# Performance work log

Measured on AMD Instinct MI355X. Metric: run time of the kernel, lower is better.

## Reference

```python
import jax, jax.numpy as jnp
import numpy as np

N_NODES = 50000


def setup_inputs() -> dict:
    key = jax.random.key(0)
    ks = jax.random.split(key, 6)
    E = 640000
    H = 128
    data = jax.random.normal(ks[0], (N_NODES, H), dtype=jnp.float32)
    edge = jax.random.randint(ks[1], (2, E), 0, N_NODES, dtype=jnp.int64)
    att = jax.random.uniform(ks[2], (E,), dtype=jnp.float32)
    w1 = jax.random.normal(ks[3], (2 * H, H), dtype=jnp.float32) * (1.0 / np.sqrt(2 * H))
    b1 = jnp.zeros((H,), dtype=jnp.float32)
    w2 = jax.random.normal(ks[4], (2 * H, H), dtype=jnp.float32) * (1.0 / np.sqrt(2 * H))
    b2 = jnp.zeros((H,), dtype=jnp.float32)
    return {"data": data, "edge": edge, "att": att, "w1": w1, "b1": b1, "w2": w2, "b2": b2}


def _simple_conv_mean_cat(x, edge, att):
    # PyG SimpleConv(aggr='mean', combine_root='cat') with scalar edge weights.
    src, dst = edge[0], edge[1]
    msgs = x[src] * att[:, None]                               # [E, H] gather + scale
    summed = jax.ops.segment_sum(msgs, dst, num_segments=N_NODES)   # [N, H]
    deg = jax.ops.segment_sum(jnp.ones_like(att), dst, num_segments=N_NODES)  # [N]
    agg = summed / jnp.maximum(deg, 1.0)[:, None]              # mean over incoming edges
    return jnp.concatenate([x, agg], axis=-1)                  # [N, 2H]


def reference(data, edge, att, w1, b1, w2, b2):
    out = _simple_conv_mean_cat(data, edge, att)
    out = jax.nn.relu(out @ w1 + b1)
    out = _simple_conv_mean_cat(out, edge, att)
    out = jax.nn.relu(out @ w2 + b2)
    return out
```

## Files before the change

### kernel.cpp

```cpp
#include <hip/hip_runtime.h>


#define HDIM 128
#define CAP 32
#define FCH 2048

typedef __bf16 bf16x8 __attribute__((ext_vector_type(8)));
typedef float floatx4 __attribute__((ext_vector_type(4)));

__device__ __forceinline__ unsigned short f2bf(float f) {
    unsigned int u = __float_as_uint(f);
    unsigned int r = (u + 0x7fff + ((u >> 16) & 1)) >> 16;
    return (unsigned short)r;
}
__device__ __forceinline__ float bf2f(unsigned short b) {
    return __uint_as_float((unsigned int)b << 16);
}

__global__ __launch_bounds__(256) void k_fill(const int* __restrict__ edge, int E,
                                              const float* __restrict__ att,
                                              int* __restrict__ cursor,
                                              int* __restrict__ ovf_cnt,
                                              unsigned int* __restrict__ pse,
                                              float4* __restrict__ ovf, int rsize,
                                              int nfb,
                                              const float* __restrict__ data,
                                              unsigned short* __restrict__ data_bf, int n4,
                                              int cb, int NN,
                                              const float* __restrict__ w1,
                                              unsigned short* __restrict__ w1t,
                                              const float* __restrict__ w2,
                                              unsigned short* __restrict__ w2t) {
    int b = blockIdx.x;
    int t = threadIdx.x;
    if (b < nfb) {
        __shared__ int s_or;
        if (t == 0) s_or = 0;
        __syncthreads();
        int nw = 2 * E < 512 ? 2 * E : 512;
        int iw = t * 2 + 1;
        int vw = (iw < nw) ? edge[iw] : 0;
        if (vw != 0) atomicOr(&s_or, 1);
        __syncthreads();
        int sh = (s_or == 0) ? 1 : 0;

        int r = b & 7;
        int c = b >> 3;
        int lo = r * rsize;
        int hi = lo + rsize;
        int e0 = c * FCH;
        int ds[8];
#pragma unroll
        for (int k = 0; k < 8; ++k) {
            int e = e0 + t + k * 256;
            ds[k] = (e < E) ? edge[(size_t)(E + e) << sh] : -1;
        }
#pragma unroll
        for (int k = 0; k < 8; ++k) {
            int d = ds[k];
            if (d >= lo && d < hi) {
                int e = e0 + t + k * 256;
                int s = edge[(size_t)e << sh];
                float a = att[e];
                int slot = atomicAdd(&cursor[d], 1);
                if (slot < CAP) {
                    unsigned int rec = ((unsigned int)f2bf(a) << 16) | (unsigned int)(s & 0xffff);
                    pse[(size_t)d * CAP + slot] = rec;
                } else {
                    int oi = atomicAdd(ovf_cnt, 1);
                    ovf[oi] = make_float4(__int_as_float(d), __int_as_float(s), a, 0.f);
                }
            }
        }
        return;
    }
    b -= nfb;
    if (b < cb) {
        int i = b * 256 + t;
        if (i < n4) {
            float4 v = ((const float4*)data)[i];
            ushort4 o;
            o.x = f2bf(v.x); o.y = f2bf(v.y); o.z = f2bf(v.z); o.w = f2bf(v.w);
            int nn = i >> 5;
            int c4 = i & 31;
            *(ushort4*)(data_bf + (((size_t)(c4 >> 3) * NN + nn) << 5) + ((c4 & 7) << 2)) = o;
        }
        return;
    }
    b -= cb;
    {
        const float* w = (b < 128) ? w1 : w2;
        unsigned short* wt = (b < 128) ? w1t : w2t;
        int bb = (b < 128) ? b : b - 128;
        int idx = bb * 256 + t;
        int k = idx >> 7;
        int n = idx & 127;
        wt[(size_t)n * 256 + k] = f2bf(w[(size_t)k * 128 + n]);
    }
}

__global__ __launch_bounds__(256) void k_agg(const unsigned short* __restrict__ x,
                                             const unsigned int* __restrict__ pse,
                                             const int* __restrict__ cursor,
                                             const int* __restrict__ ovf_cnt,
                                             const float4* __restrict__ ovf,
                                             unsigned short* __restrict__ agg, int N) {
    __shared__ __align__(16) unsigned int s_rec[64 * 36];
    int tid = threadIdx.x;
    int pass = blockIdx.y;
    int base = blockIdx.x * 64;

#pragma unroll
    for (int k = 0; k < 2; ++k) {
        int idx4 = tid + k * 256;
        int i = idx4 >> 3;
        int j0 = (idx4 & 7) << 2;
        int nn = base + i;
        uint4 v = make_uint4(0u, 0u, 0u, 0u);
        if (nn < N) v = *(const uint4*)(pse + ((size_t)nn << 5) + j0);
        *(uint4*)(&s_rec[i * 36 + j0]) = v;
    }
    __syncthreads();

    int lane = tid & 63;
    int wave = tid >> 6;
    int q = lane >> 2;
    int l4 = lane & 3;
    int ni = wave * 16 + q;
    int n = base + ni;
    bool valid = n < N;
    int deg = valid ? cursor[n] : 0;
    int m = min(deg, CAP);

    const unsigned short* xs = x + (((size_t)pass * N) << 5) + (l4 << 3);
    const unsigned int* rp = &s_rec[ni * 36];
    float s0 = 0.f, s1 = 0.f, s2 = 0.f, s3 = 0.f, s4 = 0.f, s5 = 0.f, s6 = 0.f, s7 = 0.f;

#define ACC8(u, a)                                                  \
    do {                                                            \
        s0 = fmaf(bf2f((unsigned short)((u).x & 0xffff)), (a), s0); \
        s1 = fmaf(bf2f((unsigned short)((u).x >> 16)), (a), s1);    \
        s2 = fmaf(bf2f((unsigned short)((u).y & 0xffff)), (a), s2); \
        s3 = fmaf(bf2f((unsigned short)((u).y >> 16)), (a), s3);    \
        s4 = fmaf(bf2f((unsigned short)((u).z & 0xffff)), (a), s4); \
        s5 = fmaf(bf2f((unsigned short)((u).z >> 16)), (a), s5);    \
        s6 = fmaf(bf2f((unsigned short)((u).w & 0xffff)), (a), s6); \
        s7 = fmaf(bf2f((unsigned short)((u).w >> 16)), (a), s7);    \
    } while (0)

    unsigned int rr[8];
#pragma unroll
    for (int k = 0; k < 8; ++k) {
        unsigned int r = rp[k];
        rr[k] = (k < m) ? r : 0u;
    }
    for (int j = 0; j < m; j += 8) {
        uint4 uu[8];
#pragma unroll
        for (int k = 0; k < 8; ++k)
            uu[k] = *(const uint4*)(xs + ((size_t)(rr[k] & 0xffffu) << 5));
        unsigned int rn[8];
#pragma unroll
        for (int k = 0; k < 8; ++k) {
            int jn = j + 8 + k;
            unsigned int r = (jn < m) ? rp[jn] : 0u;
            rn[k] = r;
        }
#pragma unroll
        for (int k = 0; k < 8; ++k)
            ACC8(uu[k], __uint_as_float(rr[k] & 0xffff0000u));
#pragma unroll
        for (int k = 0; k < 8; ++k) rr[k] = rn[k];
    }

    int oc = ovf_cnt[0];
    if (oc > 0 && valid) {
        for (int k = 0; k < oc; ++k) {
            float4 f = ovf[k];
            if (__float_as_int(f.x) == n) {
                uint4 u = *(const uint4*)(xs + ((size_t)__float_as_int(f.y) << 5));
                ACC8(u, f.z);
            }
        }
    }
#undef ACC8

    if (valid) {
        float inv = 1.0f / fmaxf((float)deg, 1.0f);
        uint4 o;
        o.x = (unsigned int)f2bf(s0 * inv) | ((unsigned int)f2bf(s1 * inv) << 16);
        o.y = (unsigned int)f2bf(s2 * inv) | ((unsigned int)f2bf(s3 * inv) << 16);
        o.z = (unsigned int)f2bf(s4 * inv) | ((unsigned int)f2bf(s5 * inv) << 16);
        o.w = (unsigned int)f2bf(s6 * inv) | ((unsigned int)f2bf(s7 * inv) << 16);
        *(uint4*)(agg + ((((size_t)pass * N) + n) << 5) + (l4 << 3)) = o;
    }
}

__global__ __launch_bounds__(256) void k_gemm_mfma(const unsigned short* __restrict__ X,
                                                   const unsigned short* __restrict__ AGG,
                                                   const unsigned short* __restrict__ Wt,
                                                   const float* __restrict__ bias,
                                                   float* __restrict__ outF,
                                                   unsigned short* __restrict__ outB,
                                                   int M) {
    __shared__ __align__(16) unsigned short sW[128 * 256];

    int tid = threadIdx.x;
    int wave = tid >> 6;
    int lane = tid & 63;
    int l16 = lane & 15;
    int quad = lane >> 4;

#pragma unroll
    for (int it = 0; it < 16; ++it) {
        int chunk = it * 256 + tid;
        int row = chunk >> 5;
        int c5 = chunk & 31;
        int kc = c5 >> 2;
        int q = c5 & 3;
        int qs = q ^ (row & 3);
        uint4 v = *(const uint4*)(Wt + (size_t)chunk * 8);
        *(uint4*)(sW + row * 256 + kc * 32 + qs * 8) = v;
    }

    int row = blockIdx.x * 64 + wave * 16 + l16;
    int rowA = min(row, M - 1);
    const unsigned short* xb0 = X + ((size_t)rowA << 5) + quad * 8;
    const unsigned short* ab0 = AGG + ((size_t)rowA << 5) + quad * 8;
    bf16x8 af[8];
#pragma unroll
    for (int kc = 0; kc < 4; ++kc) af[kc] = *(const bf16x8*)(xb0 + ((size_t)kc * M << 5));
#pragma unroll
    for (int kc = 0; kc < 4; ++kc) af[kc + 4] = *(const bf16x8*)(ab0 + ((size_t)kc * M << 5));

    __syncthreads();

    floatx4 acc[8];
#pragma unroll
    for (int c = 0; c < 8; ++c) acc[c] = (floatx4){0.f, 0.f, 0.f, 0.f};

#pragma unroll
    for (int kc = 0; kc < 8; ++kc) {
#pragma unroll
        for (int c = 0; c < 8; ++c) {
            int rb = c * 16 + l16;
            int qs = quad ^ (rb & 3);
            bf16x8 bfr = *(const bf16x8*)(sW + rb * 256 + kc * 32 + qs * 8);
            acc[c] = __builtin_amdgcn_mfma_f32_16x16x32_bf16(af[kc], bfr, acc[c], 0, 0, 0);
        }
    }

    int orow0 = blockIdx.x * 64 + wave * 16 + quad * 4;
#pragma unroll
    for (int c = 0; c < 8; ++c) {
        int col = c * 16 + l16;
        float bv = bias[col];
#pragma unroll
        for (int r = 0; r < 4; ++r) {
            int orow = orow0 + r;
            if (orow < M) {
                float v = fmaxf(acc[c][r] + bv, 0.f);
                if (outF) outF[(size_t)orow * 128 + col] = v;
                else outB[(((size_t)(col >> 5) * M + orow) << 5) + (col & 31)] = f2bf(v);
            }
        }
    }
}

extern "C" void kernel_launch(void* const* d_in, const int* in_sizes, int n_in,
                              void* d_out, int out_size, void* d_ws, size_t ws_size,
                              hipStream_t stream) {
    const float* data = (const float*)d_in[0];
    const int* edge = (const int*)d_in[1];
    const float* att = (const float*)d_in[2];
    const float* w1 = (const float*)d_in[3];
    const float* b1 = (const float*)d_in[4];
    const float* w2 = (const float*)d_in[5];
    const float* b2 = (const float*)d_in[6];

    const int N = in_sizes[0] / HDIM;
    const int E = in_sizes[1] / 2;

    char* ws = (char*)d_ws;
    size_t o = 0;
    auto carve = [&](size_t bytes) -> char* {
        char* r = ws + o;
        o = (o + bytes + 255) & ~(size_t)255;
        return r;
    };
    int* cursor = (int*)carve((size_t)(N + 4) * 4);
    int* ovf_cnt = cursor + N;
    unsigned int* pse = (unsigned int*)carve((size_t)N * CAP * 4);
    float4* ovf = (float4*)carve((size_t)E * 16);
    unsigned short* data_bf = (unsigned short*)carve((size_t)N * 128 * 2);
    unsigned short* w1t = (unsigned short*)carve(256 * 128 * 2);
    unsigned short* w2t = (unsigned short*)carve(256 * 128 * 2);
    unsigned short* agg_bf = (unsigned short*)carve((size_t)N * 128 * 2);
    unsigned short* out1_bf = (unsigned short*)carve((size_t)N * 128 * 2);
    float* outF = (float*)d_out;

    hipMemsetAsync(cursor, 0, (size_t)(N + 4) * 4, stream);

    int rsize = (N + 7) / 8;
    int nch = (E + FCH - 1) / FCH;
    int nfb = nch * 8;
    int n4 = N * 128 / 4;
    int cb = (n4 + 255) / 256;
    k_fill<<<nfb + cb + 256, 256, 0, stream>>>(edge, E, att, cursor, ovf_cnt, pse, ovf,
                                               rsize, nfb, data, data_bf, n4, cb, N,
                                               w1, w1t, w2, w2t);

    dim3 gag((N + 63) / 64, 4);
    int gb = (N + 63) / 64;
    k_agg<<<gag, 256, 0, stream>>>(data_bf, pse, cursor, ovf_cnt, ovf, agg_bf, N);
    k_gemm_mfma<<<gb, 256, 0, stream>>>(data_bf, agg_bf, w1t, b1, nullptr, out1_bf, N);
    k_agg<<<gag, 256, 0, stream>>>(out1_bf, pse, cursor, ovf_cnt, ovf, agg_bf, N);
    k_gemm_mfma<<<gb, 256, 0, stream>>>(out1_bf, agg_bf, w2t, b2, outF, nullptr, N);
}
```

Before: 214.2 us.

## Fuse all phases into one persistent kernel with grid barriers and work queues

Replaces the five kernel launches (fill, two aggregations, two GEMMs) with one persistent kernel of 512 blocks. The blocks take work through atomic counters and separate phases with a software grid barrier. The weights are now pre-swizzled into the MFMA fragment layout so the GEMM reads them straight from global memory instead of staging 64KB in LDS. The aggregation loops over the four feature passes inside a block rather than spreading them across grid.y. This removes launch gaps and tail effects, but the barrier relies on all 512 blocks being co-resident and reduces parallelism per phase.

```diff
diff --git a/kernel.cpp b/kernel.cpp
--- a/kernel.cpp
+++ b/kernel.cpp
@@ -4,6 +4,7 @@
 #define HDIM 128
 #define CAP 32
 #define FCH 2048
+#define NBLK 512
 
 typedef __bf16 bf16x8 __attribute__((ext_vector_type(8)));
 typedef float floatx4 __attribute__((ext_vector_type(4)));
@@ -16,255 +17,312 @@
 __device__ __forceinline__ float bf2f(unsigned short b) {
     return __uint_as_float((unsigned int)b << 16);
 }
-
-__global__ __launch_bounds__(256) void k_fill(const int* __restrict__ edge, int E,
-                                              const float* __restrict__ att,
-                                              int* __restrict__ cursor,
-                                              int* __restrict__ ovf_cnt,
-                                              unsigned int* __restrict__ pse,
-                                              float4* __restrict__ ovf, int rsize,
-                                              int nfb,
-                                              const float* __restrict__ data,
-                                              unsigned short* __restrict__ data_bf, int n4,
-                                              int cb, int NN,
-                                              const float* __restrict__ w1,
-                                              unsigned short* __restrict__ w1t,
-                                              const float* __restrict__ w2,
-                                              unsigned short* __restrict__ w2t) {
-    int b = blockIdx.x;
+__device__ __forceinline__ void acc8(const uint4& u, float a, float* s) {
+    s[0] = fmaf(bf2f((unsigned short)(u.x & 0xffff)), a, s[0]);
+    s[1] = fmaf(bf2f((unsigned short)(u.x >> 16)), a, s[1]);
+    s[2] = fmaf(bf2f((unsigned short)(u.y & 0xffff)), a, s[2]);
+    s[3] = fmaf(bf2f((unsigned short)(u.y >> 16)), a, s[3]);
+    s[4] = fmaf(bf2f((unsigned short)(u.z & 0xffff)), a, s[4]);
+    s[5] = fmaf(bf2f((unsigned short)(u.z >> 16)), a, s[5]);
+    s[6] = fmaf(bf2f((unsigned short)(u.w & 0xffff)), a, s[6]);
+    s[7] = fmaf(bf2f((unsigned short)(u.w >> 16)), a, s[7]);
+}
+
+__device__ __forceinline__ void grid_sync(int* cnt, int* gen) {
+    __syncthreads();
+    if (threadIdx.x == 0) {
+        __threadfence();
+        int g = atomicAdd(gen, 0);
+        if (atomicAdd(cnt, 1) == (int)gridDim.x - 1) {
+            atomicExch(cnt, 0);
+            __threadfence();
+            atomicAdd(gen, 1);
+        } else {
+            while (atomicAdd(gen, 0) == g) __builtin_amdgcn_s_sleep(8);
+        }
+        __threadfence();
+    }
+    __syncthreads();
+}
+
+__device__ void fill_phase(const int* __restrict__ edge, int E,
+                           const float* __restrict__ att,
+                           int* __restrict__ cursor, int* __restrict__ ovf_cnt,
+                           unsigned int* __restrict__ pse, float4* __restrict__ ovf,
+                           int rsize, int nfb,
+                           const float* __restrict__ data,
+                           unsigned short* __restrict__ data_bf, int n4, int cb, int NN,
+                           const float* __restrict__ w1, unsigned short* __restrict__ w1s,
+                           const float* __restrict__ w2, unsigned short* __restrict__ w2s,
+                           int* __restrict__ ctr) {
     int t = threadIdx.x;
-    if (b < nfb) {
-        __shared__ int s_or;
-        if (t == 0) s_or = 0;
-        __syncthreads();
+    __shared__ int s_or;
+    __shared__ int s_b;
+    if (t == 0) s_or = 0;
+    __syncthreads();
+    {
         int nw = 2 * E < 512 ? 2 * E : 512;
         int iw = t * 2 + 1;
         int vw = (iw < nw) ? edge[iw] : 0;
         if (vw != 0) atomicOr(&s_or, 1);
-        __syncthreads();
-        int sh = (s_or == 0) ? 1 : 0;
-
-        int r = b & 7;
-        int c = b >> 3;
-        int lo = r * rsize;
-        int hi = lo + rsize;
-        int e0 = c * FCH;
-        int ds[8];
-#pragma unroll
-        for (int k = 0; k < 8; ++k) {
-            int e = e0 + t + k * 256;
-            ds[k] = (e < E) ? edge[(size_t)(E + e) << sh] : -1;
-        }
-#pragma unroll
-        for (int k = 0; k < 8; ++k) {
-            int d = ds[k];
-            if (d >= lo && d < hi) {
-                int e = e0 + t + k * 256;
-                int s = edge[(size_t)e << sh];
-                float a = att[e];
-                int slot = atomicAdd(&cursor[d], 1);
-                if (slot < CAP) {
-                    unsigned int rec = ((unsigned int)f2bf(a) << 16) | (unsigned int)(s & 0xffff);
-                    pse[(size_t)d * CAP + slot] = rec;
-                } else {
-                    int oi = atomicAdd(ovf_cnt, 1);
-                    ovf[oi] = make_float4(__int_as_float(d), __int_as_float(s), a, 0.f);
-                }
-            }
-        }
-        return;
-    }
-    b -= nfb;
-    if (b < cb) {
-        int i = b * 256 + t;
-        if (i < n4) {
-            float4 v = ((const float4*)data)[i];
-            ushort4 o;
-            o.x = f2bf(v.x); o.y = f2bf(v.y); o.z = f2bf(v.z); o.w = f2bf(v.w);
-            int nn = i >> 5;
-            int c4 = i & 31;
-            *(ushort4*)(data_bf + (((size_t)(c4 >> 3) * NN + nn) << 5) + ((c4 & 7) << 2)) = o;
-        }
-        return;
-    }
-    b -= cb;
-    {
-        const float* w = (b < 128) ? w1 : w2;
-        unsigned short* wt = (b < 128) ? w1t : w2t;
-        int bb = (b < 128) ? b : b - 128;
-        int idx = bb * 256 + t;
-        int k = idx >> 7;
-        int n = idx & 127;
-        wt[(size_t)n * 256 + k] = f2bf(w[(size_t)k * 128 + n]);
-    }
-}
-
-__global__ __launch_bounds__(256) void k_agg(const unsigned short* __restrict__ x,
-                                             const unsigned int* __restrict__ pse,
-                                             const int* __restrict__ cursor,
-                                             const int* __restrict__ ovf_cnt,
-                                             const float4* __restrict__ ovf,
-                                             unsigned short* __restrict__ agg, int N) {
+    }
+    __syncthreads();
+    int sh = (s_or == 0) ? 1 : 0;
+
+    int totF = nfb + cb + 256;
+    for (;;) {
+        if (t == 0) s_b = atomicAdd(ctr, 8);
+        __syncthreads();
+        int b0 = s_b;
+        if (b0 >= totF) break;
+        int bend = min(b0 + 8, totF);
+        for (int b1 = b0; b1 < bend; ++b1) {
+            int b = b1;
+            if (b < nfb) {
+                int r = b & 7;
+                int c = b >> 3;
+                int lo = r * rsize;
+                int hi = lo + rsize;
+                int e0 = c * FCH;
+                int ds[8];
+#pragma unroll
+                for (int k = 0; k < 8; ++k) {
+                    int e = e0 + t + k * 256;
+                    ds[k] = (e < E) ? edge[(size_t)(E + e) << sh] : -1;
+                }
+#pragma unroll
+                for (int k = 0; k < 8; ++k) {
+                    int d = ds[k];
+                    if (d >= lo && d < hi) {
+                        int e = e0 + t + k * 256;
+                        int s = edge[(size_t)e << sh];
+                        float a = att[e];
+                        int slot = atomicAdd(&cursor[d], 1);
+                        if (slot < CAP) {
+                            unsigned int rec = ((unsigned int)f2bf(a) << 16) | (unsigned int)(s & 0xffff);
+                            pse[(size_t)d * CAP + slot] = rec;
+                        } else {
+                            int oi = atomicAdd(ovf_cnt, 1);
+                            ovf[oi] = make_float4(__int_as_float(d), __int_as_float(s), a, 0.f);
+                        }
+                    }
+                }
+                continue;
+            }
+            b -= nfb;
+            if (b < cb) {
+                int i = b * 256 + t;
+                if (i < n4) {
+                    float4 v = ((const float4*)data)[i];
+                    ushort4 o;
+                    o.x = f2bf(v.x); o.y = f2bf(v.y); o.z = f2bf(v.z); o.w = f2bf(v.w);
+                    int nn = i >> 5;
+                    int c4 = i & 31;
+                    *(ushort4*)(data_bf + (((size_t)(c4 >> 3) * NN + nn) << 5) + ((c4 & 7) << 2)) = o;
+                }
+                continue;
+            }
+            b -= cb;
+            {
+                const float* w = (b < 128) ? w1 : w2;
+                unsigned short* wt = (b < 128) ? w1s : w2s;
+                int bb = (b < 128) ? b : b - 128;
+                int idx = bb * 256 + t;
+                int k = idx >> 7;
+                int n = idx & 127;
+                int c = n >> 4, l16 = n & 15;
+                int kc = k >> 5, quad = (k >> 3) & 3, j = k & 7;
+                int lane = quad * 16 + l16;
+                size_t f = (((size_t)(c * 8 + kc) * 64 + lane) << 3) + j;
+                wt[f] = f2bf(w[(size_t)k * 128 + n]);
+            }
+        }
+        __syncthreads();
+    }
+}
+
+__device__ void agg_phase(const unsigned short* __restrict__ x,
+                          const unsigned int* __restrict__ pse,
+                          const int* __restrict__ cursor,
+                          const int* __restrict__ ovf_cnt,
+                          const float4* __restrict__ ovf,
+                          unsigned short* __restrict__ agg, int N,
+                          int* __restrict__ ctr) {
     __shared__ __align__(16) unsigned int s_rec[64 * 36];
+    __shared__ int s_u;
     int tid = threadIdx.x;
-    int pass = blockIdx.y;
-    int base = blockIdx.x * 64;
-
-#pragma unroll
-    for (int k = 0; k < 2; ++k) {
-        int idx4 = tid + k * 256;
-        int i = idx4 >> 3;
-        int j0 = (idx4 & 7) << 2;
-        int nn = base + i;
-        uint4 v = make_uint4(0u, 0u, 0u, 0u);
-        if (nn < N) v = *(const uint4*)(pse + ((size_t)nn << 5) + j0);
-        *(uint4*)(&s_rec[i * 36 + j0]) = v;
-    }
-    __syncthreads();
-
+    int nbk = (N + 63) >> 6;
     int lane = tid & 63;
     int wave = tid >> 6;
     int q = lane >> 2;
     int l4 = lane & 3;
-    int ni = wave * 16 + q;
-    int n = base + ni;
-    bool valid = n < N;
-    int deg = valid ? cursor[n] : 0;
-    int m = min(deg, CAP);
-
-    const unsigned short* xs = x + (((size_t)pass * N) << 5) + (l4 << 3);
-    const unsigned int* rp = &s_rec[ni * 36];
-    float s0 = 0.f, s1 = 0.f, s2 = 0.f, s3 = 0.f, s4 = 0.f, s5 = 0.f, s6 = 0.f, s7 = 0.f;
-
-#define ACC8(u, a)                                                  \
-    do {                                                            \
-        s0 = fmaf(bf2f((unsigned short)((u).x & 0xffff)), (a), s0); \
-        s1 = fmaf(bf2f((unsigned short)((u).x >> 16)), (a), s1);    \
-        s2 = fmaf(bf2f((unsigned short)((u).y & 0xffff)), (a), s2); \
-        s3 = fmaf(bf2f((unsigned short)((u).y >> 16)), (a), s3);    \
-        s4 = fmaf(bf2f((unsigned short)((u).z & 0xffff)), (a), s4); \
-        s5 = fmaf(bf2f((unsigned short)((u).z >> 16)), (a), s5);    \
-        s6 = fmaf(bf2f((unsigned short)((u).w & 0xffff)), (a), s6); \
-        s7 = fmaf(bf2f((unsigned short)((u).w >> 16)), (a), s7);    \
-    } while (0)
-
-    unsigned int rr[8];
-#pragma unroll
-    for (int k = 0; k < 8; ++k) {
-        unsigned int r = rp[k];
-        rr[k] = (k < m) ? r : 0u;
-    }
-    for (int j = 0; j < m; j += 8) {
-        uint4 uu[8];
-#pragma unroll
-        for (int k = 0; k < 8; ++k)
-            uu[k] = *(const uint4*)(xs + ((size_t)(rr[k] & 0xffffu) << 5));
-        unsigned int rn[8];
-#pragma unroll
-        for (int k = 0; k < 8; ++k) {
-            int jn = j + 8 + k;
-            unsigned int r = (jn < m) ? rp[jn] : 0u;
-            rn[k] = r;
-        }
-#pragma unroll
-        for (int k = 0; k < 8; ++k)
-            ACC8(uu[k], __uint_as_float(rr[k] & 0xffff0000u));
-#pragma unroll
-        for (int k = 0; k < 8; ++k) rr[k] = rn[k];
-    }
-
     int oc = ovf_cnt[0];
-    if (oc > 0 && valid) {
-        for (int k = 0; k < oc; ++k) {
-            float4 f = ovf[k];
-            if (__float_as_int(f.x) == n) {
-                uint4 u = *(const uint4*)(xs + ((size_t)__float_as_int(f.y) << 5));
-                ACC8(u, f.z);
-            }
-        }
-    }
-#undef ACC8
-
-    if (valid) {
+
+    for (;;) {
+        if (tid == 0) s_u = atomicAdd(ctr, 1);
+        __syncthreads();
+        int u = s_u;
+        if (u >= nbk) break;
+        int base = u * 64;
+#pragma unroll
+        for (int k = 0; k < 2; ++k) {
+            int idx4 = tid + k * 256;
+            int i = idx4 >> 3;
+            int j0 = (idx4 & 7) << 2;
+            int nn = base + i;
+            uint4 v = make_uint4(0u, 0u, 0u, 0u);
+            if (nn < N) v = *(const uint4*)(pse + ((size_t)nn << 5) + j0);
+            *(uint4*)(&s_rec[i * 36 + j0]) = v;
+        }
+        __syncthreads();
+
+        int ni = wave * 16 + q;
+        int n = base + ni;
+        bool valid = n < N;
+        int deg = valid ? cursor[n] : 0;
+        int m = min(deg, CAP);
+        const unsigned int* rp = &s_rec[ni * 36];
         float inv = 1.0f / fmaxf((float)deg, 1.0f);
-        uint4 o;
-        o.x = (unsigned int)f2bf(s0 * inv) | ((unsigned int)f2bf(s1 * inv) << 16);
-        o.y = (unsigned int)f2bf(s2 * inv) | ((unsigned int)f2bf(s3 * inv) << 16);
-        o.z = (unsigned int)f2bf(s4 * inv) | ((unsigned int)f2bf(s5 * inv) << 16);
-        o.w = (unsigned int)f2bf(s6 * inv) | ((unsigned int)f2bf(s7 * inv) << 16);
-        *(uint4*)(agg + ((((size_t)pass * N) + n) << 5) + (l4 << 3)) = o;
-    }
-}
-
-__global__ __launch_bounds__(256) void k_gemm_mfma(const unsigned short* __restrict__ X,
-                                                   const unsigned short* __restrict__ AGG,
-                                                   const unsigned short* __restrict__ Wt,
-                                                   const float* __restrict__ bias,
-                                                   float* __restrict__ outF,
-                                                   unsigned short* __restrict__ outB,
-                                                   int M) {
-    __shared__ __align__(16) unsigned short sW[128 * 256];
-
+
+        for (int pass = 0; pass < 4; ++pass) {
+            const unsigned short* xs = x + (((size_t)pass * N) << 5) + (l4 << 3);
+            float s[8] = {0.f, 0.f, 0.f, 0.f, 0.f, 0.f, 0.f, 0.f};
+
+            unsigned int rr[8];
+#pragma unroll
+            for (int k = 0; k < 8; ++k) {
+                unsigned int r = rp[k];
+                rr[k] = (k < m) ? r : 0u;
+            }
+            for (int j = 0; j < m; j += 8) {
+                uint4 uu[8];
+#pragma unroll
+                for (int k = 0; k < 8; ++k)
+                    uu[k] = *(const uint4*)(xs + ((size_t)(rr[k] & 0xffffu) << 5));
+                unsigned int rn[8];
+#pragma unroll
+                for (int k = 0; k < 8; ++k) {
+                    int jn = j + 8 + k;
+                    rn[k] = (jn < m) ? rp[jn] : 0u;
+                }
+#pragma unroll
+                for (int k = 0; k < 8; ++k)
+                    acc8(uu[k], __uint_as_float(rr[k] & 0xffff0000u), s);
+#pragma unroll
+                for (int k = 0; k < 8; ++k) rr[k] = rn[k];
+            }
+
+            if (oc > 0 && valid) {
+                for (int k = 0; k < oc; ++k) {
+                    float4 f = ovf[k];
+                    if (__float_as_int(f.x) == n) {
+                        uint4 u2 = *(const uint4*)(xs + ((size_t)__float_as_int(f.y) << 5));
+                        acc8(u2, f.z, s);
+                    }
+                }
+            }
+
+            if (valid) {
+                uint4 o;
+                o.x = (unsigned int)f2bf(s[0] * inv) | ((unsigned int)f2bf(s[1] * inv) << 16);
+                o.y = (unsigned int)f2bf(s[2] * inv) | ((unsigned int)f2bf(s[3] * inv) << 16);
+                o.z = (unsigned int)f2bf(s[4] * inv) | ((unsigned int)f2bf(s[5] * inv) << 16);
+                o.w = (unsigned int)f2bf(s[6] * inv) | ((unsigned int)f2bf(s[7] * inv) << 16);
+                *(uint4*)(agg + ((((size_t)pass * N) + n) << 5) + (l4 << 3)) = o;
+            }
+        }
+        __syncthreads();
+    }
+}
+
+__device__ void gemm_phase(const unsigned short* __restrict__ X,
+                           const unsigned short* __restrict__ AGG,
+                           const unsigned short* __restrict__ Wsw,
+                           const float* __restrict__ bias,
+                           float* __restrict__ outF,
+                           unsigned short* __restrict__ outB, int M,
+                           int* __restrict__ ctr) {
+    __shared__ int s_u;
     int tid = threadIdx.x;
     int wave = tid >> 6;
     int lane = tid & 63;
     int l16 = lane & 15;
     int quad = lane >> 4;
-
-#pragma unroll
-    for (int it = 0; it < 16; ++it) {
-        int chunk = it * 256 + tid;
-        int row = chunk >> 5;
-        int c5 = chunk & 31;
-        int kc = c5 >> 2;
-        int q = c5 & 3;
-        int qs = q ^ (row & 3);
-        uint4 v = *(const uint4*)(Wt + (size_t)chunk * 8);
-        *(uint4*)(sW + row * 256 + kc * 32 + qs * 8) = v;
-    }
-
-    int row = blockIdx.x * 64 + wave * 16 + l16;
-    int rowA = min(row, M - 1);
-    const unsigned short* xb0 = X + ((size_t)rowA << 5) + quad * 8;
-    const unsigned short* ab0 = AGG + ((size_t)rowA << 5) + quad * 8;
-    bf16x8 af[8];
-#pragma unroll
-    for (int kc = 0; kc < 4; ++kc) af[kc] = *(const bf16x8*)(xb0 + ((size_t)kc * M << 5));
-#pragma unroll
-    for (int kc = 0; kc < 4; ++kc) af[kc + 4] = *(const bf16x8*)(ab0 + ((size_t)kc * M << 5));
-
-    __syncthreads();
-
-    floatx4 acc[8];
-#pragma unroll
-    for (int c = 0; c < 8; ++c) acc[c] = (floatx4){0.f, 0.f, 0.f, 0.f};
-
-#pragma unroll
-    for (int kc = 0; kc < 8; ++kc) {
+    int nbk = (M + 63) >> 6;
+
+    for (;;) {
+        if (tid == 0) s_u = atomicAdd(ctr, 1);
+        __syncthreads();
+        int u = s_u;
+        if (u >= nbk) break;
+
+        int row = u * 64 + wave * 16 + l16;
+        int rowA = min(row, M - 1);
+        const unsigned short* xb0 = X + ((size_t)rowA << 5) + quad * 8;
+        const unsigned short* ab0 = AGG + ((size_t)rowA << 5) + quad * 8;
+        bf16x8 af[8];
+#pragma unroll
+        for (int kc = 0; kc < 4; ++kc) af[kc] = *(const bf16x8*)(xb0 + (((size_t)kc * M) << 5));
+#pragma unroll
+        for (int kc = 0; kc < 4; ++kc) af[kc + 4] = *(const bf16x8*)(ab0 + (((size_t)kc * M) << 5));
+
+        floatx4 acc[8];
+#pragma unroll
+        for (int c = 0; c < 8; ++c) acc[c] = (floatx4){0.f, 0.f, 0.f, 0.f};
+
+#pragma unroll
+        for (int kc = 0; kc < 8; ++kc) {
+#pragma unroll
+            for (int c = 0; c < 8; ++c) {
+                bf16x8 bfr = *(const bf16x8*)(Wsw + (((size_t)(c * 8 + kc) * 64 + lane) << 3));
+                acc[c] = __builtin_amdgcn_mfma_f32_16x16x32_bf16(af[kc], bfr, acc[c], 0, 0, 0);
+            }
+        }
+
+        int orow0 = u * 64 + wave * 16 + quad * 4;
 #pragma unroll
         for (int c = 0; c < 8; ++c) {
-            int rb = c * 16 + l16;
-            int qs = quad ^ (rb & 3);
-            bf16x8 bfr = *(const bf16x8*)(sW + rb * 256 + kc * 32 + qs * 8);
-            acc[c] = __builtin_amdgcn_mfma_f32_16x16x32_bf16(af[kc], bfr, acc[c], 0, 0, 0);
-        }
-    }
-
-    int orow0 = blockIdx.x * 64 + wave * 16 + quad * 4;
-#pragma unroll
-    for (int c = 0; c < 8; ++c) {
-        int col = c * 16 + l16;
-        float bv = bias[col];
-#pragma unroll
-        for (int r = 0; r < 4; ++r) {
-            int orow = orow0 + r;
-            if (orow < M) {
-                float v = fmaxf(acc[c][r] + bv, 0.f);
-                if (outF) outF[(size_t)orow * 128 + col] = v;
-                else outB[(((size_t)(col >> 5) * M + orow) << 5) + (col & 31)] = f2bf(v);
-            }
-        }
-    }
+            int col = c * 16 + l16;
+            float bv = bias[col];
+#pragma unroll
+            for (int r = 0; r < 4; ++r) {
+                int orow = orow0 + r;
+                if (orow < M) {
+                    float v = fmaxf(acc[c][r] + bv, 0.f);
+                    if (outF) outF[(size_t)orow * 128 + col] = v;
+                    else outB[(((size_t)(col >> 5) * M + orow) << 5) + (col & 31)] = f2bf(v);
+                }
+            }
+        }
+        __syncthreads();
+    }
+}
+
+__global__ __launch_bounds__(256, 2) void k_mega(const int* edge, int E, const float* att,
+                                                 int* cursor, int* ovf_cnt,
+                                                 unsigned int* pse, float4* ovf,
+                                                 int rsize, int nfb,
+                                                 const float* data, unsigned short* data_bf,
+                                                 int n4, int cb, int N,
+                                                 const float* w1, unsigned short* w1s,
+                                                 const float* w2, unsigned short* w2s,
+                                                 const float* b1, const float* b2,
+                                                 unsigned short* agg_bf, unsigned short* out1_bf,
+                                                 float* outF, int* bar, int* wk) {
+    fill_phase(edge, E, att, cursor, ovf_cnt, pse, ovf, rsize, nfb,
+               data, data_bf, n4, cb, N, w1, w1s, w2, w2s, &wk[0]);
+    grid_sync(&bar[0], &bar[1]);
+
+    agg_phase(data_bf, pse, cursor, ovf_cnt, ovf, agg_bf, N, &wk[1]);
+    grid_sync(&bar[0], &bar[1]);
+
+    gemm_phase(data_bf, agg_bf, w1s, b1, nullptr, out1_bf, N, &wk[2]);
+    grid_sync(&bar[0], &bar[1]);
+
+    agg_phase(out1_bf, pse, cursor, ovf_cnt, ovf, agg_bf, N, &wk[3]);
+    grid_sync(&bar[0], &bar[1]);
+
+    gemm_phase(out1_bf, agg_bf, w2s, b2, outF, nullptr, N, &wk[4]);
 }
 
 extern "C" void kernel_launch(void* const* d_in, const int* in_sizes, int n_in,
@@ -278,8 +336,8 @@
     const float* w2 = (const float*)d_in[5];
     const float* b2 = (const float*)d_in[6];
 
-    const int N = in_sizes[0] / HDIM;
-    const int E = in_sizes[1] / 2;
+    int N = in_sizes[0] / HDIM;
+    int E = in_sizes[1] / 2;
 
     char* ws = (char*)d_ws;
     size_t o = 0;
@@ -288,32 +346,29 @@
         o = (o + bytes + 255) & ~(size_t)255;
         return r;
     };
-    int* cursor = (int*)carve((size_t)(N + 4) * 4);
+    int* cursor = (int*)carve((size_t)(N + 16) * 4);
     int* ovf_cnt = cursor + N;
+    int* bar = cursor + N + 4;
+    int* wk = cursor + N + 8;
     unsigned int* pse = (unsigned int*)carve((size_t)N * CAP * 4);
     float4* ovf = (float4*)carve((size_t)E * 16);
     unsigned short* data_bf = (unsigned short*)carve((size_t)N * 128 * 2);
-    unsigned short* w1t = (unsigned short*)carve(256 * 128 * 2);
-    unsigned short* w2t = (unsigned short*)carve(256 * 128 * 2);
+    unsigned short* w1s = (unsigned short*)carve(256 * 128 * 2);
+    unsigned short* w2s = (unsigned short*)carve(256 * 128 * 2);
     unsigned short* agg_bf = (unsigned short*)carve((size_t)N * 128 * 2);
     unsigned short* out1_bf = (unsigned short*)carve((size_t)N * 128 * 2);
     float* outF = (float*)d_out;
 
-    hipMemsetAsync(cursor, 0, (size_t)(N + 4) * 4, stream);
+    hipMemsetAsync(cursor, 0, (size_t)(N + 16) * 4, stream);
 
     int rsize = (N + 7) / 8;
     int nch = (E + FCH - 1) / FCH;
     int nfb = nch * 8;
-    int n4 = N * 128 / 4;
+    int n4 = N * 32;
     int cb = (n4 + 255) / 256;
-    k_fill<<<nfb + cb + 256, 256, 0, stream>>>(edge, E, att, cursor, ovf_cnt, pse, ovf,
-                                               rsize, nfb, data, data_bf, n4, cb, N,
-                                               w1, w1t, w2, w2t);
-
-    dim3 gag((N + 63) / 64, 4);
-    int gb = (N + 63) / 64;
-    k_agg<<<gag, 256, 0, stream>>>(data_bf, pse, cursor, ovf_cnt, ovf, agg_bf, N);
-    k_gemm_mfma<<<gb, 256, 0, stream>>>(data_bf, agg_bf, w1t, b1, nullptr, out1_bf, N);
-    k_agg<<<gag, 256, 0, stream>>>(out1_bf, pse, cursor, ovf_cnt, ovf, agg_bf, N);
-    k_gemm_mfma<<<gb, 256, 0, stream>>>(out1_bf, agg_bf, w2t, b2, outF, nullptr, N);
-}
+
+    k_mega<<<dim3(NBLK), dim3(256), 0, stream>>>(edge, E, att, cursor, ovf_cnt, pse, ovf,
+                                                 rsize, nfb, data, data_bf, n4, cb, N,
+                                                 w1, w1s, w2, w2s, b1, b2,
+                                                 agg_bf, out1_bf, outF, bar, wk);
+}
```

Measured after the change: 637.2 us. 197% more time.

## Fuse aggregation and MFMA GEMM into one per-layer kernel with pre-swizzled weights

Applied to the files above, without the earlier changes.

Merges the aggregation kernel and the GEMM kernel into a single k_layer kernel. Each block aggregates all four 32-column passes for its 64 nodes into shared memory and feeds them straight into the MFMA GEMM, so the agg_bf round trip through global memory and two launches are gone. Weights are now pre-swizzled into the MFMA fragment layout during k_fill and read directly from global/L2 rather than staged through a 64KB LDS tile. The gather loop also batches 16 neighbours at a time. In exchange, the grid drops from 4x to 1x node blocks, so there is less parallelism for hiding gather latency, and every block re-reads the weights from cache.

```diff
diff --git a/kernel.cpp b/kernel.cpp
--- a/kernel.cpp
+++ b/kernel.cpp
@@ -15,6 +15,16 @@
 }
 __device__ __forceinline__ float bf2f(unsigned short b) {
     return __uint_as_float((unsigned int)b << 16);
+}
+__device__ __forceinline__ void acc8(const uint4& u, float a, float* s) {
+    s[0] = fmaf(bf2f((unsigned short)(u.x & 0xffff)), a, s[0]);
+    s[1] = fmaf(bf2f((unsigned short)(u.x >> 16)), a, s[1]);
+    s[2] = fmaf(bf2f((unsigned short)(u.y & 0xffff)), a, s[2]);
+    s[3] = fmaf(bf2f((unsigned short)(u.y >> 16)), a, s[3]);
+    s[4] = fmaf(bf2f((unsigned short)(u.z & 0xffff)), a, s[4]);
+    s[5] = fmaf(bf2f((unsigned short)(u.z >> 16)), a, s[5]);
+    s[6] = fmaf(bf2f((unsigned short)(u.w & 0xffff)), a, s[6]);
+    s[7] = fmaf(bf2f((unsigned short)(u.w >> 16)), a, s[7]);
 }
 
 __global__ __launch_bounds__(256) void k_fill(const int* __restrict__ edge, int E,
@@ -28,9 +38,9 @@
                                               unsigned short* __restrict__ data_bf, int n4,
                                               int cb, int NN,
                                               const float* __restrict__ w1,
-                                              unsigned short* __restrict__ w1t,
+                                              unsigned short* __restrict__ w1s,
                                               const float* __restrict__ w2,
-                                              unsigned short* __restrict__ w2t) {
+                                              unsigned short* __restrict__ w2s) {
     int b = blockIdx.x;
     int t = threadIdx.x;
     if (b < nfb) {
@@ -90,24 +100,32 @@
     b -= cb;
     {
         const float* w = (b < 128) ? w1 : w2;
-        unsigned short* wt = (b < 128) ? w1t : w2t;
+        unsigned short* wt = (b < 128) ? w1s : w2s;
         int bb = (b < 128) ? b : b - 128;
         int idx = bb * 256 + t;
         int k = idx >> 7;
         int n = idx & 127;
-        wt[(size_t)n * 256 + k] = f2bf(w[(size_t)k * 128 + n]);
-    }
-}
-
-__global__ __launch_bounds__(256) void k_agg(const unsigned short* __restrict__ x,
-                                             const unsigned int* __restrict__ pse,
-                                             const int* __restrict__ cursor,
-                                             const int* __restrict__ ovf_cnt,
-                                             const float4* __restrict__ ovf,
-                                             unsigned short* __restrict__ agg, int N) {
+        int c = n >> 4, l16 = n & 15;
+        int kc = k >> 5, quad = (k >> 3) & 3, j = k & 7;
+        int lane = quad * 16 + l16;
+        size_t f = (((size_t)(c * 8 + kc) * 64 + lane) << 3) + j;
+        wt[f] = f2bf(w[(size_t)k * 128 + n]);
+    }
+}
+
+__global__ __launch_bounds__(256, 4) void k_layer(const unsigned short* __restrict__ x,
+                                                  const unsigned int* __restrict__ pse,
+                                                  const int* __restrict__ cursor,
+                                                  const int* __restrict__ ovf_cnt,
+                                                  const float4* __restrict__ ovf,
+                                                  const unsigned short* __restrict__ Wsw,
+                                                  const float* __restrict__ bias,
+                                                  float* __restrict__ outF,
+                                                  unsigned short* __restrict__ outB,
+                                                  int M) {
     __shared__ __align__(16) unsigned int s_rec[64 * 36];
+    __shared__ __align__(16) unsigned short s_agg[64 * 136];
     int tid = threadIdx.x;
-    int pass = blockIdx.y;
     int base = blockIdx.x * 64;
 
 #pragma unroll
@@ -117,7 +135,7 @@
         int j0 = (idx4 & 7) << 2;
         int nn = base + i;
         uint4 v = make_uint4(0u, 0u, 0u, 0u);
-        if (nn < N) v = *(const uint4*)(pse + ((size_t)nn << 5) + j0);
+        if (nn < M) v = *(const uint4*)(pse + ((size_t)nn << 5) + j0);
         *(uint4*)(&s_rec[i * 36 + j0]) = v;
     }
     __syncthreads();
@@ -128,112 +146,64 @@
     int l4 = lane & 3;
     int ni = wave * 16 + q;
     int n = base + ni;
-    bool valid = n < N;
+    bool valid = n < M;
     int deg = valid ? cursor[n] : 0;
     int m = min(deg, CAP);
-
-    const unsigned short* xs = x + (((size_t)pass * N) << 5) + (l4 << 3);
     const unsigned int* rp = &s_rec[ni * 36];
-    float s0 = 0.f, s1 = 0.f, s2 = 0.f, s3 = 0.f, s4 = 0.f, s5 = 0.f, s6 = 0.f, s7 = 0.f;
-
-#define ACC8(u, a)                                                  \
-    do {                                                            \
-        s0 = fmaf(bf2f((unsigned short)((u).x & 0xffff)), (a), s0); \
-        s1 = fmaf(bf2f((unsigned short)((u).x >> 16)), (a), s1);    \
-        s2 = fmaf(bf2f((unsigned short)((u).y & 0xffff)), (a), s2); \
-        s3 = fmaf(bf2f((unsigned short)((u).y >> 16)), (a), s3);    \
-        s4 = fmaf(bf2f((unsigned short)((u).z & 0xffff)), (a), s4); \
-        s5 = fmaf(bf2f((unsigned short)((u).z >> 16)), (a), s5);    \
-        s6 = fmaf(bf2f((unsigned short)((u).w & 0xffff)), (a), s6); \
-        s7 = fmaf(bf2f((unsigned short)((u).w >> 16)), (a), s7);    \
-    } while (0)
-
-    unsigned int rr[8];
-#pragma unroll
-    for (int k = 0; k < 8; ++k) {
-        unsigned int r = rp[k];
-        rr[k] = (k < m) ? r : 0u;
-    }
-    for (int j = 0; j < m; j += 8) {
-        uint4 uu[8];
-#pragma unroll
-        for (int k = 0; k < 8; ++k)
-            uu[k] = *(const uint4*)(xs + ((size_t)(rr[k] & 0xffffu) << 5));
-        unsigned int rn[8];
-#pragma unroll
-        for (int k = 0; k < 8; ++k) {
-            int jn = j + 8 + k;
-            unsigned int r = (jn < m) ? rp[jn] : 0u;
-            rn[k] = r;
-        }
-#pragma unroll
-        for (int k = 0; k < 8; ++k)
-            ACC8(uu[k], __uint_as_float(rr[k] & 0xffff0000u));
-#pragma unroll
-        for (int k = 0; k < 8; ++k) rr[k] = rn[k];
-    }
-
+    float inv = 1.0f / fmaxf((float)deg, 1.0f);
     int oc = ovf_cnt[0];
-    if (oc > 0 && valid) {
-        for (int k = 0; k < oc; ++k) {
-            float4 f = ovf[k];
-            if (__float_as_int(f.x) == n) {
-                uint4 u = *(const uint4*)(xs + ((size_t)__float_as_int(f.y) << 5));
-                ACC8(u, f.z);
-            }
-        }
-    }
-#undef ACC8
-
-    if (valid) {
-        float inv = 1.0f / fmaxf((float)deg, 1.0f);
+
+    for (int pass = 0; pass < 4; ++pass) {
+        const unsigned short* xs = x + (((size_t)pass * M) << 5) + (l4 << 3);
+        float s[8] = {0.f, 0.f, 0.f, 0.f, 0.f, 0.f, 0.f, 0.f};
+
+        for (int j = 0; j < m; j += 16) {
+            unsigned int rr[16];
+#pragma unroll
+            for (int k = 0; k < 16; ++k) {
+                unsigned int r = rp[j + k];
+                rr[k] = (j + k < m) ? r : 0u;
+            }
+            uint4 uu[16];
+#pragma unroll
+            for (int k = 0; k < 16; ++k)
+                uu[k] = *(const uint4*)(xs + ((size_t)(rr[k] & 0xffffu) << 5));
+#pragma unroll
+            for (int k = 0; k < 16; ++k)
+                acc8(uu[k], __uint_as_float(rr[k] & 0xffff0000u), s);
+        }
+
+        if (oc > 0 && valid) {
+            for (int k = 0; k < oc; ++k) {
+                float4 f = ovf[k];
+                if (__float_as_int(f.x) == n) {
+                    uint4 u2 = *(const uint4*)(xs + ((size_t)__float_as_int(f.y) << 5));
+                    acc8(u2, f.z, s);
+                }
+            }
+        }
+
         uint4 o;
-        o.x = (unsigned int)f2bf(s0 * inv) | ((unsigned int)f2bf(s1 * inv) << 16);
-        o.y = (unsigned int)f2bf(s2 * inv) | ((unsigned int)f2bf(s3 * inv) << 16);
-        o.z = (unsigned int)f2bf(s4 * inv) | ((unsigned int)f2bf(s5 * inv) << 16);
-        o.w = (unsigned int)f2bf(s6 * inv) | ((unsigned int)f2bf(s7 * inv) << 16);
-        *(uint4*)(agg + ((((size_t)pass * N) + n) << 5) + (l4 << 3)) = o;
-    }
-}
-
-__global__ __launch_bounds__(256) void k_gemm_mfma(const unsigned short* __restrict__ X,
-                                                   const unsigned short* __restrict__ AGG,
-                                                   const unsigned short* __restrict__ Wt,
-                                                   const float* __restrict__ bias,
-                                                   float* __restrict__ outF,
-                                                   unsigned short* __restrict__ outB,
-                                                   int M) {
-    __shared__ __align__(16) unsigned short sW[128 * 256];
-
-    int tid = threadIdx.x;
-    int wave = tid >> 6;
-    int lane = tid & 63;
+        o.x = (unsigned int)f2bf(s[0] * inv) | ((unsigned int)f2bf(s[1] * inv) << 16);
+        o.y = (unsigned int)f2bf(s[2] * inv) | ((unsigned int)f2bf(s[3] * inv) << 16);
+        o.z = (unsigned int)f2bf(s[4] * inv) | ((unsigned int)f2bf(s[5] * inv) << 16);
+        o.w = (unsigned int)f2bf(s[6] * inv) | ((unsigned int)f2bf(s[7] * inv) << 16);
+        *(uint4*)(&s_agg[ni * 136 + pass * 32 + l4 * 8]) = o;
+    }
+    __syncthreads();
+
     int l16 = lane & 15;
     int quad = lane >> 4;
-
-#pragma unroll
-    for (int it = 0; it < 16; ++it) {
-        int chunk = it * 256 + tid;
-        int row = chunk >> 5;
-        int c5 = chunk & 31;
-        int kc = c5 >> 2;
-        int q = c5 & 3;
-        int qs = q ^ (row & 3);
-        uint4 v = *(const uint4*)(Wt + (size_t)chunk * 8);
-        *(uint4*)(sW + row * 256 + kc * 32 + qs * 8) = v;
-    }
-
-    int row = blockIdx.x * 64 + wave * 16 + l16;
+    int row = base + wave * 16 + l16;
     int rowA = min(row, M - 1);
-    const unsigned short* xb0 = X + ((size_t)rowA << 5) + quad * 8;
-    const unsigned short* ab0 = AGG + ((size_t)rowA << 5) + quad * 8;
+    int lrow = wave * 16 + l16;
+    const unsigned short* xb0 = x + ((size_t)rowA << 5) + quad * 8;
     bf16x8 af[8];
 #pragma unroll
-    for (int kc = 0; kc < 4; ++kc) af[kc] = *(const bf16x8*)(xb0 + ((size_t)kc * M << 5));
-#pragma unroll
-    for (int kc = 0; kc < 4; ++kc) af[kc + 4] = *(const bf16x8*)(ab0 + ((size_t)kc * M << 5));
-
-    __syncthreads();
+    for (int kc = 0; kc < 4; ++kc) af[kc] = *(const bf16x8*)(xb0 + (((size_t)kc * M) << 5));
+#pragma unroll
+    for (int kc = 0; kc < 4; ++kc)
+        af[kc + 4] = *(const bf16x8*)(&s_agg[lrow * 136 + kc * 32 + quad * 8]);
 
     floatx4 acc[8];
 #pragma unroll
@@ -243,14 +213,12 @@
     for (int kc = 0; kc < 8; ++kc) {
 #pragma unroll
         for (int c = 0; c < 8; ++c) {
-            int rb = c * 16 + l16;
-            int qs = quad ^ (rb & 3);
-            bf16x8 bfr = *(const bf16x8*)(sW + rb * 256 + kc * 32 + qs * 8);
+            bf16x8 bfr = *(const bf16x8*)(Wsw + (((size_t)(c * 8 + kc) * 64 + lane) << 3));
             acc[c] = __builtin_amdgcn_mfma_f32_16x16x32_bf16(af[kc], bfr, acc[c], 0, 0, 0);
         }
     }
 
-    int orow0 = blockIdx.x * 64 + wave * 16 + quad * 4;
+    int orow0 = base + wave * 16 + quad * 4;
 #pragma unroll
     for (int c = 0; c < 8; ++c) {
         int col = c * 16 + l16;
@@ -293,9 +261,8 @@
     unsigned int* pse = (unsigned int*)carve((size_t)N * CAP * 4);
     float4* ovf = (float4*)carve((size_t)E * 16);
     unsigned short* data_bf = (unsigned short*)carve((size_t)N * 128 * 2);
-    unsigned short* w1t = (unsigned short*)carve(256 * 128 * 2);
-    unsigned short* w2t = (unsigned short*)carve(256 * 128 * 2);
-    unsigned short* agg_bf = (unsigned short*)carve((size_t)N * 128 * 2);
+    unsigned short* w1s = (unsigned short*)carve(256 * 128 * 2);
+    unsigned short* w2s = (unsigned short*)carve(256 * 128 * 2);
     unsigned short* out1_bf = (unsigned short*)carve((size_t)N * 128 * 2);
     float* outF = (float*)d_out;
 
@@ -304,16 +271,15 @@
     int rsize = (N + 7) / 8;
     int nch = (E + FCH - 1) / FCH;
     int nfb = nch * 8;
-    int n4 = N * 128 / 4;
+    int n4 = N * 32;
     int cb = (n4 + 255) / 256;
     k_fill<<<nfb + cb + 256, 256, 0, stream>>>(edge, E, att, cursor, ovf_cnt, pse, ovf,
                                                rsize, nfb, data, data_bf, n4, cb, N,
-                                               w1, w1t, w2, w2t);
-
-    dim3 gag((N + 63) / 64, 4);
-    int gb = (N + 63) / 64;
-    k_agg<<<gag, 256, 0, stream>>>(data_bf, pse, cursor, ovf_cnt, ovf, agg_bf, N);
-    k_gemm_mfma<<<gb, 256, 0, stream>>>(data_bf, agg_bf, w1t, b1, nullptr, out1_bf, N);
-    k_agg<<<gag, 256, 0, stream>>>(out1_bf, pse, cursor, ovf_cnt, ovf, agg_bf, N);
-    k_gemm_mfma<<<gb, 256, 0, stream>>>(out1_bf, agg_bf, w2t, b2, outF, nullptr, N);
-}
+                                               w1, w1s, w2, w2s);
+
+    int nbk = (N + 63) / 64;
+    k_layer<<<nbk, 256, 0, stream>>>(data_bf, pse, cursor, ovf_cnt, ovf,
+                                     w1s, b1, nullptr, out1_bf, N);
+    k_layer<<<nbk, 256, 0, stream>>>(out1_bf, pse, cursor, ovf_cnt, ovf,
+                                     w2s, b2, outF, nullptr, N);
+}
```

After: 206.1 us. 1.04x faster.
